# Optimization experiments

Measured on AMD Instinct MI355X. Metric: run time of the kernel, lower is better.

## Reference

```python
import jax, jax.numpy as jnp
import numpy as np

N = 1_000_000
D_IN = 128
D_OUT = 64
NUM_CLASSES = 64


def setup_inputs() -> dict:
    key = jax.random.key(0)
    k1, k2, k3, k4 = jax.random.split(key, 4)
    inputs = jax.random.normal(k1, (N, D_IN), dtype=jnp.float32)
    labels = jax.random.randint(k2, (N,), 0, NUM_CLASSES, dtype=jnp.int32)
    # Linear embedding parameters
    W = jax.random.normal(k3, (D_IN, D_OUT), dtype=jnp.float32) / np.sqrt(D_IN)
    b = jax.random.normal(k4, (D_OUT,), dtype=jnp.float32) * 0.01
    return {"inputs": inputs, "labels": labels, "W": W, "b": b}


def reference(inputs, labels, W, b):
    # embedding: simple linear map  [N, D_IN] -> [N, D_OUT]
    emb = jnp.einsum("nd,de->ne", inputs, W) + b
    # per-class mean pooling (prototype): segment sum / segment count
    seg_sum = jax.ops.segment_sum(emb, labels, num_segments=NUM_CLASSES)  # [C, D_OUT]
    counts = jax.ops.segment_sum(jnp.ones((inputs.shape[0],), dtype=emb.dtype),
                                 labels, num_segments=NUM_CLASSES)  # [C]
    protos = seg_sum / jnp.maximum(counts, 1.0)[:, None]
    return protos
```

## Files before the change

### kernel.cpp

```cpp
#include <hip/hip_runtime.h>

#define C_CLASSES 64
#define D_IN 128
#define D_OUT 64
#define CHUNK 32
#define CHUNK_FLTS (CHUNK * D_IN)
#define GSUM_FLTS (C_CLASSES * D_IN)
#define NBLK 1024


typedef __attribute__((ext_vector_type(8))) __bf16 bf16x8;
typedef __attribute__((ext_vector_type(8))) unsigned short us8;
typedef __attribute__((ext_vector_type(4))) float f32x4;

union frag_cast { us8 u; bf16x8 b; };

__device__ __forceinline__ unsigned short f2bf(float f) {
    unsigned u = __float_as_uint(f);
    unsigned r = u + 0x7FFFu + ((u >> 16) & 1u);
    return (unsigned short)(r >> 16);
}

__device__ __forceinline__ void stage16(const float* g, float* l) {
    __builtin_amdgcn_global_load_lds(
        (const __attribute__((address_space(1))) unsigned int*)g,
        (__attribute__((address_space(3))) unsigned int*)l, 16, 0, 0);
}

__global__ __launch_bounds__(256) void seg_mm_kernel(
    const float* __restrict__ x, const int* __restrict__ labels,
    float* __restrict__ gsum, int n)
{
    __shared__ float buf[2][CHUNK_FLTS];

    const int lane = threadIdx.x & 63;
    const int wave = threadIdx.x >> 6;
    const int n16  = lane & 15;
    const int quad = lane >> 4;
    const int cb   = wave * 32;
    const int xu   = quad & 1;

    f32x4 acc[4][2];
#pragma unroll
    for (int t = 0; t < 4; ++t)
#pragma unroll
        for (int u = 0; u < 2; ++u)
            acc[t][u] = (f32x4){0.f, 0.f, 0.f, 0.f};

    const int stride = (int)gridDim.x * CHUNK;
    const int rb0    = (int)blockIdx.x * CHUNK;
    const int lslice = wave * 256;

    int goff[4];
#pragma unroll
    for (int r = 0; r < 4; ++r) {
        const int o = r * 1024 + lslice + lane * 4;
        const int k = o >> 7;
        const int d = o & 127;
        goff[r] = k * D_IN + (d ^ (((k >> 3) & 1) << 4));
    }

    int4 pl0 = {0,0,0,0}, pl1 = {0,0,0,0};
    if (rb0 < n) {
#pragma unroll
        for (int r = 0; r < 4; ++r)
            stage16(x + (size_t)rb0 * D_IN + goff[r],
                    &buf[0][r * 1024 + lslice]);
        pl0 = *(const int4*)(labels + rb0 + quad * 8);
        pl1 = *(const int4*)(labels + rb0 + quad * 8 + 4);
    }

    int bufi = 0;
    for (int rb = rb0; rb < n; rb += stride, bufi ^= 1) {
        const int rbn = rb + stride;
        const bool hasNext = rbn < n;
        int4 pn0, pn1;
        if (hasNext) {
#pragma unroll
            for (int r = 0; r < 4; ++r)
                stage16(x + (size_t)rbn * D_IN + goff[r],
                        &buf[bufi ^ 1][r * 1024 + lslice]);
            pn0 = *(const int4*)(labels + rbn + quad * 8);
            pn1 = *(const int4*)(labels + rbn + quad * 8 + 4);
        }

        if (hasNext) {
            asm volatile("s_waitcnt vmcnt(6)\n\ts_barrier" ::: "memory");
        } else {
            asm volatile("s_waitcnt vmcnt(0)\n\ts_barrier" ::: "memory");
        }

        const int labv[8] = {pl0.x, pl0.y, pl0.z, pl0.w,
                             pl1.x, pl1.y, pl1.z, pl1.w};

        const float* lb = &buf[bufi][(quad * 8) * D_IN + cb + n16];
        frag_cast bfrag[2];
#pragma unroll
        for (int u = 0; u < 2; ++u)
#pragma unroll
            for (int j = 0; j < 8; ++j)
                bfrag[u].u[j] = f2bf(lb[j * D_IN + ((u ^ xu) * 16)]);

        frag_cast afrag[4];
#pragma unroll
        for (int t = 0; t < 4; ++t)
#pragma unroll
            for (int j = 0; j < 8; ++j)
                afrag[t].u[j] = (labv[j] == t * 16 + n16)
                                    ? (unsigned short)0x3F80u : (unsigned short)0u;

#pragma unroll
        for (int t = 0; t < 4; ++t)
#pragma unroll
            for (int u = 0; u < 2; ++u)
                acc[t][u] = __builtin_amdgcn_mfma_f32_16x16x32_bf16(
                    afrag[t].b, bfrag[u].b, acc[t][u], 0, 0, 0);

        asm volatile("s_barrier" ::: "memory");

        if (hasNext) { pl0 = pn0; pl1 = pn1; }
    }

#pragma unroll
    for (int t = 0; t < 4; ++t)
#pragma unroll
        for (int u = 0; u < 2; ++u)
#pragma unroll
            for (int r = 0; r < 4; ++r)
                unsafeAtomicAdd(
                    &gsum[(t * 16 + quad * 4 + r) * D_IN + cb + u * 16 + n16],
                    acc[t][u][r]);
}

__global__ __launch_bounds__(256) void count_kernel(
    const int* __restrict__ labels, float* __restrict__ gcnt, int n)
{
    const int lane = threadIdx.x & 63;
    const int gw   = (int)(blockIdx.x * blockDim.x + threadIdx.x) >> 6;
    const int nw   = (int)(gridDim.x * blockDim.x) >> 6;

    int cnt = 0;
    for (int base = gw * 64; base < n; base += nw * 64) {
        const int lab = labels[base + lane];
#pragma unroll
        for (int c = 0; c < C_CLASSES; ++c) {
            unsigned long long m = __ballot(lab == c);
            cnt += (lane == c) ? __popcll(m) : 0;
        }
    }
    unsafeAtomicAdd(&gcnt[lane], (float)cnt);
}

__global__ __launch_bounds__(256) void proto_kernel(
    const float* __restrict__ gsum, const float* __restrict__ gcnt,
    const float* __restrict__ W, const float* __restrict__ b,
    float* __restrict__ out)
{
    const int t = (int)(blockIdx.x * blockDim.x + threadIdx.x);
    const int c = t >> 6;
    const int e = t & 63;

    const float* srow = gsum + (c << 7);
    float acc = 0.0f;
#pragma unroll
    for (int k = 0; k < D_IN; ++k)
        acc = fmaf(srow[k], W[k * D_OUT + e], acc);

    const float cnt = gcnt[c];
    out[(c << 6) + e] = (acc + cnt * b[e]) / fmaxf(cnt, 1.0f);
}

extern "C" void kernel_launch(void* const* d_in, const int* in_sizes, int n_in,
                              void* d_out, int out_size, void* d_ws, size_t ws_size,
                              hipStream_t stream)
{
    const float* x      = (const float*)d_in[0];
    const int*   labels = (const int*)d_in[1];
    const float* W      = (const float*)d_in[2];
    const float* b      = (const float*)d_in[3];
    float*       out    = (float*)d_out;

    float* gsum = (float*)d_ws;
    float* gcnt = gsum + GSUM_FLTS;

    const int n = in_sizes[0] / D_IN;

    hipMemsetAsync(d_ws, 0, (GSUM_FLTS + C_CLASSES) * sizeof(float), stream);

    seg_mm_kernel<<<NBLK, 256, 0, stream>>>(x, labels, gsum, n);

    count_kernel<<<1024, 256, 0, stream>>>(labels, gcnt, n);

    proto_kernel<<<(C_CLASSES * D_OUT) / 256, 256, 0, stream>>>(gsum, gcnt, W, b, out);
}
```

Measured before the change: 764.2 us.

## Fuse class counting into MFMA kernel and replace atomics with partial-sum reduction

After: 683.1 us. 1.12x faster.

```diff
diff --git a/kernel.cpp b/kernel.cpp
--- a/kernel.cpp
+++ b/kernel.cpp
@@ -29,7 +29,7 @@
 
 __global__ __launch_bounds__(256) void seg_mm_kernel(
     const float* __restrict__ x, const int* __restrict__ labels,
-    float* __restrict__ gsum, int n)
+    float* __restrict__ partials, float* __restrict__ cnt_p, int n)
 {
     __shared__ float buf[2][CHUNK_FLTS];
 
@@ -41,11 +41,18 @@
     const int xu   = quad & 1;
 
     f32x4 acc[4][2];
-#pragma unroll
-    for (int t = 0; t < 4; ++t)
+    f32x4 acc_cnt[4];
+#pragma unroll
+    for (int t = 0; t < 4; ++t) {
+        acc_cnt[t] = (f32x4){0.f, 0.f, 0.f, 0.f};
 #pragma unroll
         for (int u = 0; u < 2; ++u)
             acc[t][u] = (f32x4){0.f, 0.f, 0.f, 0.f};
+    }
+
+    frag_cast ones;
+#pragma unroll
+    for (int j = 0; j < 8; ++j) ones.u[j] = (unsigned short)0x3F80u;
 
     const int stride = (int)gridDim.x * CHUNK;
     const int rb0    = (int)blockIdx.x * CHUNK;
@@ -60,15 +67,12 @@
         goff[r] = k * D_IN + (d ^ (((k >> 3) & 1) << 4));
     }
 
-    int4 pl0 = {0,0,0,0}, pl1 = {0,0,0,0};
-    if (rb0 < n) {
-#pragma unroll
-        for (int r = 0; r < 4; ++r)
-            stage16(x + (size_t)rb0 * D_IN + goff[r],
-                    &buf[0][r * 1024 + lslice]);
-        pl0 = *(const int4*)(labels + rb0 + quad * 8);
-        pl1 = *(const int4*)(labels + rb0 + quad * 8 + 4);
-    }
+#pragma unroll
+    for (int r = 0; r < 4; ++r)
+        stage16(x + (size_t)rb0 * D_IN + goff[r],
+                &buf[0][r * 1024 + lslice]);
+    int4 pl0 = *(const int4*)(labels + rb0 + quad * 8);
+    int4 pl1 = *(const int4*)(labels + rb0 + quad * 8 + 4);
 
     int bufi = 0;
     for (int rb = rb0; rb < n; rb += stride, bufi ^= 1) {
@@ -110,49 +114,76 @@
                                     ? (unsigned short)0x3F80u : (unsigned short)0u;
 
 #pragma unroll
-        for (int t = 0; t < 4; ++t)
+        for (int t = 0; t < 4; ++t) {
 #pragma unroll
             for (int u = 0; u < 2; ++u)
                 acc[t][u] = __builtin_amdgcn_mfma_f32_16x16x32_bf16(
                     afrag[t].b, bfrag[u].b, acc[t][u], 0, 0, 0);
+            acc_cnt[t] = __builtin_amdgcn_mfma_f32_16x16x32_bf16(
+                afrag[t].b, ones.b, acc_cnt[t], 0, 0, 0);
+        }
 
         asm volatile("s_barrier" ::: "memory");
 
         if (hasNext) { pl0 = pn0; pl1 = pn1; }
     }
 
+    float* pT = partials + (size_t)blockIdx.x * GSUM_FLTS;
 #pragma unroll
     for (int t = 0; t < 4; ++t)
 #pragma unroll
-        for (int u = 0; u < 2; ++u)
-#pragma unroll
-            for (int r = 0; r < 4; ++r)
-                unsafeAtomicAdd(
-                    &gsum[(t * 16 + quad * 4 + r) * D_IN + cb + u * 16 + n16],
-                    acc[t][u][r]);
-}
-
-__global__ __launch_bounds__(256) void count_kernel(
-    const int* __restrict__ labels, float* __restrict__ gcnt, int n)
-{
-    const int lane = threadIdx.x & 63;
-    const int gw   = (int)(blockIdx.x * blockDim.x + threadIdx.x) >> 6;
-    const int nw   = (int)(gridDim.x * blockDim.x) >> 6;
-
-    int cnt = 0;
-    for (int base = gw * 64; base < n; base += nw * 64) {
-        const int lab = labels[base + lane];
-#pragma unroll
-        for (int c = 0; c < C_CLASSES; ++c) {
-            unsigned long long m = __ballot(lab == c);
-            cnt += (lane == c) ? __popcll(m) : 0;
-        }
-    }
-    unsafeAtomicAdd(&gcnt[lane], (float)cnt);
+        for (int u = 0; u < 2; ++u) {
+            const int col = cb + u * 16 + n16;
+            *(f32x4*)&pT[col * C_CLASSES + t * 16 + quad * 4] = acc[t][u];
+        }
+
+    if (wave == 0 && n16 == 0) {
+        float* cp = cnt_p + (size_t)blockIdx.x * C_CLASSES;
+#pragma unroll
+        for (int t = 0; t < 4; ++t)
+            *(f32x4*)&cp[t * 16 + quad * 4] = acc_cnt[t];
+    }
+}
+
+__global__ __launch_bounds__(256) void reduce_kernel(
+    const float* __restrict__ partials, const float* __restrict__ cnt_p,
+    float* __restrict__ gsumT, float* __restrict__ gcnt)
+{
+    __shared__ float red[256];
+    const int b = (int)blockIdx.x;
+    const int t = (int)threadIdx.x;
+
+    if (b < 256) {
+        const int s   = b * 32 + (t & 31);
+        const int oct = t >> 5;
+        float a = 0.f;
+#pragma unroll 8
+        for (int p = oct * 128; p < oct * 128 + 128; ++p)
+            a += partials[(size_t)p * GSUM_FLTS + s];
+        red[t] = a;
+        __syncthreads();
+        if (oct == 0) {
+            float v = 0.f;
+#pragma unroll
+            for (int o = 0; o < 8; ++o) v += red[o * 32 + t];
+            gsumT[s] = v;
+        }
+    } else {
+        const int c = t & 63;
+        const int q = t >> 6;
+        float a = 0.f;
+#pragma unroll 8
+        for (int p = q * 256; p < q * 256 + 256; ++p)
+            a += cnt_p[(size_t)p * C_CLASSES + c];
+        red[t] = a;
+        __syncthreads();
+        if (q == 0)
+            gcnt[c] = red[c] + red[64 + c] + red[128 + c] + red[192 + c];
+    }
 }
 
 __global__ __launch_bounds__(256) void proto_kernel(
-    const float* __restrict__ gsum, const float* __restrict__ gcnt,
+    const float* __restrict__ gsumT, const float* __restrict__ gcnt,
     const float* __restrict__ W, const float* __restrict__ b,
     float* __restrict__ out)
 {
@@ -160,11 +191,10 @@
     const int c = t >> 6;
     const int e = t & 63;
 
-    const float* srow = gsum + (c << 7);
     float acc = 0.0f;
 #pragma unroll
     for (int k = 0; k < D_IN; ++k)
-        acc = fmaf(srow[k], W[k * D_OUT + e], acc);
+        acc = fmaf(gsumT[k * C_CLASSES + c], W[k * D_OUT + e], acc);
 
     const float cnt = gcnt[c];
     out[(c << 6) + e] = (acc + cnt * b[e]) / fmaxf(cnt, 1.0f);
@@ -180,16 +210,18 @@
     const float* b      = (const float*)d_in[3];
     float*       out    = (float*)d_out;
 
-    float* gsum = (float*)d_ws;
-    float* gcnt = gsum + GSUM_FLTS;
+    float* gsumT    = (float*)d_ws;
+    float* gcnt     = gsumT + GSUM_FLTS;
+    float* partials = gcnt + C_CLASSES;
+    float* cnt_p    = partials + (size_t)NBLK * GSUM_FLTS;
 
     const int n = in_sizes[0] / D_IN;
 
-    hipMemsetAsync(d_ws, 0, (GSUM_FLTS + C_CLASSES) * sizeof(float), stream);
-
-    seg_mm_kernel<<<NBLK, 256, 0, stream>>>(x, labels, gsum, n);
-
-    count_kernel<<<1024, 256, 0, stream>>>(labels, gcnt, n);
-
-    proto_kernel<<<(C_CLASSES * D_OUT) / 256, 256, 0, stream>>>(gsum, gcnt, W, b, out);
-}
+
+    seg_mm_kernel<<<NBLK, 256, 0, stream>>>(x, labels, partials, cnt_p, n);
+
+    reduce_kernel<<<257, 256, 0, stream>>>(partials, cnt_p, gsumT, gcnt);
+
+    proto_kernel<<<(C_CLASSES * D_OUT) / 256, 256, 0, stream>>>(
+        gsumT, gcnt, W, b, out);
+}
```
